# Performance work log

Measured on AMD Instinct MI355X. Metric: run time of the kernel, lower is better.

Reference implementation:

```python
import jax, jax.numpy as jnp
import numpy as np

N = 50000      # nodes
E = 400000     # edges per meta-path
P = 3          # meta-paths
H = 4          # attention heads
D = 32         # hidden_size per head
IN = 128       # in_size = 86 + 42
HD = H * D     # 128
NEG_SLOPE = 0.2


def setup_inputs() -> dict:
    key = jax.random.key(0)
    ks = jax.random.split(key, 13)
    return {
        "h": jax.random.normal(ks[0], (N, 86), dtype=jnp.float32),
        "c_ineigh_feature": jax.random.normal(ks[1], (N, 20, 42), dtype=jnp.float32),
        "fa_w1": jax.random.normal(ks[2], (42, 16), dtype=jnp.float32) * 0.1,
        "fa_b1": jnp.zeros((16,), dtype=jnp.float32),
        "fa_w2": jax.random.normal(ks[3], (16, 1), dtype=jnp.float32) * 0.1,
        "gat_W": jax.random.normal(ks[4], (P, IN, HD), dtype=jnp.float32) * 0.05,
        "attn_l": jax.random.normal(ks[5], (P, H, D), dtype=jnp.float32) * 0.1,
        "attn_r": jax.random.normal(ks[6], (P, H, D), dtype=jnp.float32) * 0.1,
        "sa_w1": jax.random.normal(ks[7], (HD, 128), dtype=jnp.float32) * 0.1,
        "sa_b1": jnp.zeros((128,), dtype=jnp.float32),
        "sa_w2": jax.random.normal(ks[8], (128, 1), dtype=jnp.float32) * 0.1,
        "src": jax.random.randint(ks[9], (P, E), 0, N, dtype=jnp.int32),
        "dst": jax.random.randint(ks[10], (P, E), 0, N, dtype=jnp.int32),
    }


def _gat_conv(x, W, a_l, a_r, s, d):
    """DGL-style GATConv (feat_drop=attn_drop=0, eval mode), activation=elu."""
    feat = (x @ W).reshape(N, H, D)               # [N,H,D]
    el = (feat * a_l).sum(-1)                     # [N,H]
    er = (feat * a_r).sum(-1)                     # [N,H]
    e = el[s] + er[d]                             # [E,H]
    e = jnp.where(e > 0, e, NEG_SLOPE * e)        # leaky_relu(0.2)
    # edge softmax over incoming edges of each dst node
    m = jax.ops.segment_max(e, d, num_segments=N)
    m = jax.lax.stop_gradient(jnp.where(jnp.isfinite(m), m, 0.0))
    ee = jnp.exp(e - m[d])                        # [E,H]
    z = jax.ops.segment_sum(ee, d, num_segments=N)
    alpha = ee / z[d]                             # [E,H]
    msg = alpha[:, :, None] * feat[s]             # [E,H,D]
    out = jax.ops.segment_sum(msg, d, num_segments=N)  # [N,H,D]
    return jax.nn.elu(out).reshape(N, HD)


def reference(h, c_ineigh_feature, fa_w1, fa_b1, fa_w2, gat_W, attn_l, attn_r,
              sa_w1, sa_b1, sa_w2, src, dst):
    # FeatureAttention over the 42-dim neighbor features
    w = jnp.tanh(c_ineigh_feature @ fa_w1 + fa_b1) @ fa_w2   # [N,20,1]
    beta = jax.nn.softmax(w, axis=1)
    c_emb = (beta * c_ineigh_feature).sum(1)                 # [N,42]
    x = jnp.concatenate([h, c_emb], axis=1)                  # [N,128]

    # One GATConv per meta-path
    embs = [_gat_conv(x, gat_W[p], attn_l[p], attn_r[p], src[p], dst[p])
            for p in range(P)]
    z = jnp.stack(embs, axis=1)                              # [N,P,HD]

    # SemanticAttention across meta-paths
    wsem = (jnp.tanh(z @ sa_w1 + sa_b1) @ sa_w2).mean(0)     # [P,1]
    bsem = jax.nn.softmax(wsem, axis=0)                      # [P,1]
    return (bsem[None] * z).sum(1)                           # [N,HD]
```

## Files before the change

### kernel.cpp

```cpp
#include <hip/hip_runtime.h>
#include <hip/hip_bf16.h>

#define NN 50000
#define EE 400000
#define PP 3
#define NBLK 196

__device__ __forceinline__ float eluf(float v) {
    return v > 0.f ? v : (expf(v) - 1.f);
}

__device__ __forceinline__ void fma4(float4& a, float s, const float4& w) {
    a.x += s * w.x; a.y += s * w.y; a.z += s * w.z; a.w += s * w.w;
}

__device__ __forceinline__ unsigned short f2bf(float f) {
    unsigned int u = __float_as_uint(f);
    u = (u + 0x7FFFu + ((u >> 16) & 1u)) >> 16;
    return (unsigned short)u;
}
__device__ __forceinline__ float bf_lo(unsigned int u) { return __uint_as_float(u << 16); }
__device__ __forceinline__ float bf_hi(unsigned int u) { return __uint_as_float(u & 0xFFFF0000u); }

__global__ __launch_bounds__(256) void k_fa_w(
    const float* __restrict__ c, const float* __restrict__ w1,
    const float* __restrict__ b1, const float* __restrict__ w2,
    float* __restrict__ wout)
{
    __shared__ float sW1[42 * 16];
    const int tid = threadIdx.x;
    for (int i = tid; i < 672; i += 256) sW1[i] = w1[i];
    __syncthreads();

    const int t = blockIdx.x * 256 + tid;
    if (t >= NN * 5) return;
    const int n = t / 5;
    const int q = t - 5 * n;

    const float2* base = (const float2*)(c + (size_t)n * 840 + q * 168);
    const float4* sW4 = (const float4*)sW1;

    float4 acc[4][4];
    #pragma unroll
    for (int r = 0; r < 4; ++r)
        #pragma unroll
        for (int jq = 0; jq < 4; ++jq) acc[r][jq] = make_float4(0.f, 0.f, 0.f, 0.f);

    #pragma unroll 3
    for (int i2 = 0; i2 < 21; ++i2) {
        const float4 wa0 = sW4[(2 * i2) * 4 + 0];
        const float4 wa1 = sW4[(2 * i2) * 4 + 1];
        const float4 wa2 = sW4[(2 * i2) * 4 + 2];
        const float4 wa3 = sW4[(2 * i2) * 4 + 3];
        const float4 wb0 = sW4[(2 * i2 + 1) * 4 + 0];
        const float4 wb1 = sW4[(2 * i2 + 1) * 4 + 1];
        const float4 wb2 = sW4[(2 * i2 + 1) * 4 + 2];
        const float4 wb3 = sW4[(2 * i2 + 1) * 4 + 3];
        #pragma unroll
        for (int r = 0; r < 4; ++r) {
            const float2 v = base[r * 21 + i2];
            fma4(acc[r][0], v.x, wa0); fma4(acc[r][1], v.x, wa1);
            fma4(acc[r][2], v.x, wa2); fma4(acc[r][3], v.x, wa3);
            fma4(acc[r][0], v.y, wb0); fma4(acc[r][1], v.y, wb1);
            fma4(acc[r][2], v.y, wb2); fma4(acc[r][3], v.y, wb3);
        }
    }

    float4 bb[4], ww[4];
    #pragma unroll
    for (int jq = 0; jq < 4; ++jq) {
        bb[jq] = ((const float4*)b1)[jq];
        ww[jq] = ((const float4*)w2)[jq];
    }
    float* wo = wout + (size_t)n * 20 + q * 4;
    #pragma unroll
    for (int r = 0; r < 4; ++r) {
        float s = 0.f;
        #pragma unroll
        for (int jq = 0; jq < 4; ++jq) {
            s += tanhf(acc[r][jq].x + bb[jq].x) * ww[jq].x;
            s += tanhf(acc[r][jq].y + bb[jq].y) * ww[jq].y;
            s += tanhf(acc[r][jq].z + bb[jq].z) * ww[jq].z;
            s += tanhf(acc[r][jq].w + bb[jq].w) * ww[jq].w;
        }
        wo[r] = s;
    }
}

__global__ __launch_bounds__(256) void k_fa_emb(
    const float* __restrict__ h, const float* __restrict__ c,
    const float* __restrict__ w, float* __restrict__ x)
{
    const int wid = threadIdx.x >> 6, lane = threadIdx.x & 63;
    const int n = blockIdx.x * 4 + wid;
    if (n >= NN) return;

    const float* wn = w + (size_t)n * 20;
    float wv[20];
    #pragma unroll
    for (int r = 0; r < 20; ++r) wv[r] = wn[r];
    float m = wv[0];
    #pragma unroll
    for (int r = 1; r < 20; ++r) m = fmaxf(m, wv[r]);
    float s = 0.f;
    #pragma unroll
    for (int r = 0; r < 20; ++r) { wv[r] = expf(wv[r] - m); s += wv[r]; }
    const float inv = 1.f / s;

    if (lane < 42) {
        const float* cn = c + (size_t)n * 840;
        float acc = 0.f;
        #pragma unroll
        for (int r = 0; r < 20; ++r) acc += wv[r] * cn[r * 42 + lane];
        x[(size_t)n * 128 + 86 + lane] = acc * inv;
    }
    x[(size_t)n * 128 + lane] = h[(size_t)n * 86 + lane];
    if (lane < 22)
        x[(size_t)n * 128 + 64 + lane] = h[(size_t)n * 86 + 64 + lane];
}

__global__ __launch_bounds__(256) void k_gat_gemm(
    const float* __restrict__ x, const float* __restrict__ W,
    const float* __restrict__ attn_l, const float* __restrict__ attn_r,
    unsigned short* __restrict__ featb, float* __restrict__ el, float* __restrict__ er)
{
    __shared__ float sX[64 * 128];
    const int tid = threadIdx.x;
    const int p  = blockIdx.y;
    const int n0 = blockIdx.x * 64;

    float4* sX4 = (float4*)sX;
    for (int i = tid; i < 2048; i += 256) {
        const int row = i >> 5, c4 = i & 31;
        float4 v = make_float4(0.f, 0.f, 0.f, 0.f);
        if (n0 + row < NN) v = ((const float4*)(x + (size_t)(n0 + row) * 128))[c4];
        sX4[i] = v;
    }
    __syncthreads();

    const int tc = tid & 31;
    const int tr = tid >> 5;
    const float4* Wp4 = (const float4*)(W + (size_t)p * 128 * 128);

    float4 acc[8];
    #pragma unroll
    for (int r = 0; r < 8; ++r) acc[r] = make_float4(0.f, 0.f, 0.f, 0.f);

    for (int kq = 0; kq < 32; ++kq) {
        const float4 wv0 = Wp4[(4 * kq + 0) * 32 + tc];
        const float4 wv1 = Wp4[(4 * kq + 1) * 32 + tc];
        const float4 wv2 = Wp4[(4 * kq + 2) * 32 + tc];
        const float4 wv3 = Wp4[(4 * kq + 3) * 32 + tc];
        #pragma unroll
        for (int r = 0; r < 8; ++r) {
            const float4 xv = sX4[(tr * 8 + r) * 32 + kq];
            fma4(acc[r], xv.x, wv0);
            fma4(acc[r], xv.y, wv1);
            fma4(acc[r], xv.z, wv2);
            fma4(acc[r], xv.w, wv3);
        }
    }

    float4 al, ar;
    {
        al = ((const float4*)(attn_l + p * 128))[tc];
        ar = ((const float4*)(attn_r + p * 128))[tc];
    }
    const int hh = tc >> 3;
    for (int r = 0; r < 8; ++r) {
        const int n = n0 + tr * 8 + r;
        const bool ok = n < NN;
        if (ok) {
            ushort4 sv;
            sv.x = f2bf(acc[r].x); sv.y = f2bf(acc[r].y);
            sv.z = f2bf(acc[r].z); sv.w = f2bf(acc[r].w);
            ((ushort4*)(featb + (size_t)(p * NN + n) * 128))[tc] = sv;
        }
        float pl = acc[r].x*al.x + acc[r].y*al.y + acc[r].z*al.z + acc[r].w*al.w;
        float pr = acc[r].x*ar.x + acc[r].y*ar.y + acc[r].z*ar.z + acc[r].w*ar.w;
        pl += __shfl_xor(pl, 1); pl += __shfl_xor(pl, 2); pl += __shfl_xor(pl, 4);
        pr += __shfl_xor(pr, 1); pr += __shfl_xor(pr, 2); pr += __shfl_xor(pr, 4);
        if (ok && (tc & 7) == 0) {
            el[(size_t)(p * NN + n) * 4 + hh] = pl;
            er[(size_t)(p * NN + n) * 4 + hh] = pr;
        }
    }
}

__global__ __launch_bounds__(256) void k_hist(
    const int* __restrict__ dst, int* __restrict__ deg)
{
    const int p = blockIdx.y;
    const int e = blockIdx.x * 256 + threadIdx.x;
    if (e < EE) atomicAdd(&deg[p * NN + dst[p * EE + e]], 1);
}

__global__ __launch_bounds__(256) void k_partial(
    const int* __restrict__ deg, int* __restrict__ psum)
{
    __shared__ int s[256];
    const int p = blockIdx.y;
    const int i = blockIdx.x * 256 + threadIdx.x;
    s[threadIdx.x] = (i < NN) ? deg[p * NN + i] : 0;
    __syncthreads();
    for (int off = 128; off > 0; off >>= 1) {
        if (threadIdx.x < off) s[threadIdx.x] += s[threadIdx.x + off];
        __syncthreads();
    }
    if (threadIdx.x == 0) psum[p * NBLK + blockIdx.x] = s[0];
}

__global__ void k_scanpsum(int* __restrict__ psum)
{
    const int p = blockIdx.x;
    if (threadIdx.x == 0) {
        int run = 0;
        for (int i = 0; i < NBLK; ++i) {
            int t = psum[p * NBLK + i];
            psum[p * NBLK + i] = run;
            run += t;
        }
    }
}

__global__ __launch_bounds__(256) void k_scanfinal(
    const int* __restrict__ deg, const int* __restrict__ psum,
    int* __restrict__ row_start, int* __restrict__ cursor)
{
    __shared__ int s[256];
    const int p = blockIdx.y, t = threadIdx.x;
    const int i = blockIdx.x * 256 + t;
    const int v = (i < NN) ? deg[p * NN + i] : 0;
    s[t] = v;
    __syncthreads();
    for (int off = 1; off < 256; off <<= 1) {
        int xv = 0;
        if (t >= off) xv = s[t - off];
        __syncthreads();
        s[t] += xv;
        __syncthreads();
    }
    const int excl = s[t] - v + psum[p * NBLK + blockIdx.x];
    if (i < NN) {
        row_start[p * (NN + 1) + i] = excl;
        cursor[p * NN + i] = excl;
        if (i == NN - 1) row_start[p * (NN + 1) + NN] = excl + v;
    }
}

__global__ __launch_bounds__(256) void k_scatter(
    const int* __restrict__ src, const int* __restrict__ dst,
    const float* __restrict__ el, const float* __restrict__ er,
    int* __restrict__ cursor, int* __restrict__ s_src, float* __restrict__ s_ee)
{
    const int p = blockIdx.y;
    const int e = blockIdx.x * 256 + threadIdx.x;
    if (e >= EE) return;
    const int s = src[p * EE + e];
    const int d = dst[p * EE + e];
    const float4 a = ((const float4*)el)[p * NN + s];
    const float4 b = ((const float4*)er)[p * NN + d];
    float4 o;
    {
        float t0 = a.x + b.x, t1 = a.y + b.y, t2 = a.z + b.z, t3 = a.w + b.w;
        t0 = t0 > 0.f ? t0 : 0.2f * t0;
        t1 = t1 > 0.f ? t1 : 0.2f * t1;
        t2 = t2 > 0.f ? t2 : 0.2f * t2;
        t3 = t3 > 0.f ? t3 : 0.2f * t3;
        o = make_float4(expf(t0), expf(t1), expf(t2), expf(t3));
    }
    const int slot = atomicAdd(&cursor[p * NN + d], 1);
    s_src[p * EE + slot] = s;
    ((float4*)s_ee)[p * EE + slot] = o;
}

__global__ __launch_bounds__(256) void k_agg(
    const int* __restrict__ row_start, const int* __restrict__ s_src,
    const float* __restrict__ s_ee, const unsigned short* __restrict__ featb,
    unsigned int* __restrict__ zb)
{
    const int p = blockIdx.y;
    const int w = threadIdx.x >> 6;
    const int lane = threadIdx.x & 63;
    const int n = blockIdx.x * 4 + w;
    if (n >= NN) return;
    const int st = row_start[p * (NN + 1) + n];
    const int en = row_start[p * (NN + 1) + n + 1];

    const int h = lane >> 4;
    const int* ss = s_src + (size_t)p * EE;
    const float4* ee4 = (const float4*)s_ee + (size_t)p * EE;
    const unsigned short* fbase = featb + (size_t)p * NN * 128;

    float acc0 = 0.f, acc1 = 0.f, za = 0.f;
    int i = st;
    for (; i + 4 <= en; i += 4) {
        const int sn0 = ss[i], sn1 = ss[i + 1], sn2 = ss[i + 2], sn3 = ss[i + 3];
        const float4 q0 = ee4[i], q1 = ee4[i + 1], q2 = ee4[i + 2], q3 = ee4[i + 3];
        const unsigned int u0 = ((const unsigned int*)(fbase + (size_t)sn0 * 128))[lane];
        const unsigned int u1 = ((const unsigned int*)(fbase + (size_t)sn1 * 128))[lane];
        const unsigned int u2 = ((const unsigned int*)(fbase + (size_t)sn2 * 128))[lane];
        const unsigned int u3 = ((const unsigned int*)(fbase + (size_t)sn3 * 128))[lane];
        const float e0 = (h < 2) ? (h == 0 ? q0.x : q0.y) : (h == 2 ? q0.z : q0.w);
        const float e1 = (h < 2) ? (h == 0 ? q1.x : q1.y) : (h == 2 ? q1.z : q1.w);
        const float e2 = (h < 2) ? (h == 0 ? q2.x : q2.y) : (h == 2 ? q2.z : q2.w);
        const float e3 = (h < 2) ? (h == 0 ? q3.x : q3.y) : (h == 2 ? q3.z : q3.w);
        acc0 += e0 * bf_lo(u0) + e1 * bf_lo(u1) + e2 * bf_lo(u2) + e3 * bf_lo(u3);
        acc1 += e0 * bf_hi(u0) + e1 * bf_hi(u1) + e2 * bf_hi(u2) + e3 * bf_hi(u3);
        za += (e0 + e1) + (e2 + e3);
    }
    for (; i < en; ++i) {
        const int sn = ss[i];
        const float4 q = ee4[i];
        const unsigned int u = ((const unsigned int*)(fbase + (size_t)sn * 128))[lane];
        const float e = (h < 2) ? (h == 0 ? q.x : q.y) : (h == 2 ? q.z : q.w);
        acc0 += e * bf_lo(u);
        acc1 += e * bf_hi(u);
        za += e;
    }
    float v0 = 0.f, v1 = 0.f;
    if (en > st) { const float iz = 1.f / za; v0 = acc0 * iz; v1 = acc1 * iz; }
    v0 = v0 > 0.f ? v0 : (expf(v0) - 1.f);
    v1 = v1 > 0.f ? v1 : (expf(v1) - 1.f);
    zb[(size_t)(p * NN + n) * 64 + lane] =
        (unsigned int)f2bf(v0) | ((unsigned int)f2bf(v1) << 16);
}

__global__ __launch_bounds__(256) void k_sem_score(
    const unsigned int* __restrict__ zb, const float* __restrict__ w1,
    const float* __restrict__ b1, const float* __restrict__ w2,
    float* __restrict__ wsem)
{
    __shared__ float sZ[64 * 128];
    __shared__ float sPart[8];
    const int tid = threadIdx.x;
    const int p  = blockIdx.y;
    const int n0 = blockIdx.x * 64;

    float4* sZ4 = (float4*)sZ;
    for (int i = tid; i < 2048; i += 256) {
        const int row = i >> 5, c4 = i & 31;
        float4 v = make_float4(0.f, 0.f, 0.f, 0.f);
        if (n0 + row < NN) {
            const uint2 u = ((const uint2*)(zb + (size_t)(p * NN + n0 + row) * 64))[c4];
            v.x = bf_lo(u.x); v.y = bf_hi(u.x); v.z = bf_lo(u.y); v.w = bf_hi(u.y);
        }
        sZ4[i] = v;
    }
    __syncthreads();

    const int tc = tid & 31;
    const int tr = tid >> 5;
    const float4* w14 = (const float4*)w1;

    float4 acc[8];
    #pragma unroll
    for (int r = 0; r < 8; ++r) acc[r] = make_float4(0.f, 0.f, 0.f, 0.f);

    for (int kq = 0; kq < 32; ++kq) {
        const float4 wv0 = w14[(4 * kq + 0) * 32 + tc];
        const float4 wv1 = w14[(4 * kq + 1) * 32 + tc];
        const float4 wv2 = w14[(4 * kq + 2) * 32 + tc];
        const float4 wv3 = w14[(4 * kq + 3) * 32 + tc];
        #pragma unroll
        for (int r = 0; r < 8; ++r) {
            const float4 zv = sZ4[(tr * 8 + r) * 32 + kq];
            fma4(acc[r], zv.x, wv0);
            fma4(acc[r], zv.y, wv1);
            fma4(acc[r], zv.z, wv2);
            fma4(acc[r], zv.w, wv3);
        }
    }

    const float4 bb = ((const float4*)b1)[tc];
    const float4 ww = ((const float4*)w2)[tc];

    float local = 0.f;
    for (int r = 0; r < 8; ++r) {
        float pr = tanhf(acc[r].x + bb.x) * ww.x
                 + tanhf(acc[r].y + bb.y) * ww.y
                 + tanhf(acc[r].z + bb.z) * ww.z
                 + tanhf(acc[r].w + bb.w) * ww.w;
        pr += __shfl_xor(pr, 1);
        pr += __shfl_xor(pr, 2);
        pr += __shfl_xor(pr, 4);
        pr += __shfl_xor(pr, 8);
        pr += __shfl_xor(pr, 16);
        if (tc == 0 && (n0 + tr * 8 + r) < NN) local += pr;
    }
    if (tc == 0) sPart[tr] = local;
    __syncthreads();
    if (tid == 0) {
        float t = 0.f;
        for (int i = 0; i < 8; ++i) t += sPart[i];
        atomicAdd(&wsem[p], t);
    }
}

__global__ void k_bsem(const float* __restrict__ wsem, float* __restrict__ bsem)
{
    if (threadIdx.x == 0 && blockIdx.x == 0) {
        float w[PP];
        for (int p = 0; p < PP; ++p) w[p] = wsem[p] / (float)NN;
        float m = fmaxf(w[0], fmaxf(w[1], w[2]));
        float s = 0.f;
        for (int p = 0; p < PP; ++p) { w[p] = expf(w[p] - m); s += w[p]; }
        for (int p = 0; p < PP; ++p) bsem[p] = w[p] / s;
    }
}

__global__ __launch_bounds__(256) void k_final(
    const unsigned int* __restrict__ zb, const float* __restrict__ bsem,
    float* __restrict__ out)
{
    const int i = blockIdx.x * 256 + threadIdx.x;
    if (i >= NN * 64) return;
    const float b0 = bsem[0], b1 = bsem[1], b2 = bsem[2];
    const unsigned int u0 = zb[i];
    const unsigned int u1 = zb[(size_t)NN * 64 + i];
    const unsigned int u2 = zb[(size_t)2 * NN * 64 + i];
    float2 o;
    o.x = b0 * bf_lo(u0) + b1 * bf_lo(u1) + b2 * bf_lo(u2);
    o.y = b0 * bf_hi(u0) + b1 * bf_hi(u1) + b2 * bf_hi(u2);
    ((float2*)out)[i] = o;
}

extern "C" void kernel_launch(void* const* d_in, const int* in_sizes, int n_in,
                              void* d_out, int out_size, void* d_ws, size_t ws_size,
                              hipStream_t stream) {
    const float* h      = (const float*)d_in[0];
    const float* c      = (const float*)d_in[1];
    const float* fa_w1  = (const float*)d_in[2];
    const float* fa_b1  = (const float*)d_in[3];
    const float* fa_w2  = (const float*)d_in[4];
    const float* gat_W  = (const float*)d_in[5];
    const float* attn_l = (const float*)d_in[6];
    const float* attn_r = (const float*)d_in[7];
    const float* sa_w1  = (const float*)d_in[8];
    const float* sa_b1  = (const float*)d_in[9];
    const float* sa_w2  = (const float*)d_in[10];
    const int*   src    = (const int*)d_in[11];
    const int*   dst    = (const int*)d_in[12];
    float* out = (float*)d_out;

    float* ws = (float*)d_ws;
    float* x     = ws;
    int*   s_src = (int*)ws;
    float* s_ee  = ws + 1200000;
    float* w_fa  = ws + 6400000;
    unsigned short* featb = (unsigned short*)(ws + 7400000);
    float* el    = ws + 17000000;
    float* er    = el + 600000;
    unsigned int* zb = (unsigned int*)(er + 600000);
    int*   row_start = (int*)(ws + 27800000);
    int*   cursor    = row_start + 150003;
    int*   psum      = cursor + 150000;
    int*   deg       = psum + 588;
    float* wsem      = (float*)(deg + 150000);
    float* bsem      = wsem + 4;

    hipMemsetAsync(deg, 0, (size_t)(150000 + 4) * sizeof(float), stream);

    k_fa_w<<<(NN * 5 + 255) / 256, 256, 0, stream>>>(c, fa_w1, fa_b1, fa_w2, w_fa);
    k_fa_emb<<<(NN + 3) / 4, 256, 0, stream>>>(h, c, w_fa, x);
    k_gat_gemm<<<dim3((NN + 63) / 64, PP), 256, 0, stream>>>(x, gat_W, attn_l, attn_r, featb, el, er);
    k_hist<<<dim3((EE + 255) / 256, PP), 256, 0, stream>>>(dst, deg);
    k_partial<<<dim3(NBLK, PP), 256, 0, stream>>>(deg, psum);
    k_scanpsum<<<PP, 64, 0, stream>>>(psum);
    k_scanfinal<<<dim3(NBLK, PP), 256, 0, stream>>>(deg, psum, row_start, cursor);
    k_scatter<<<dim3((EE + 255) / 256, PP), 256, 0, stream>>>(src, dst, el, er, cursor, s_src, s_ee);
    k_agg<<<dim3((NN + 3) / 4, PP), 256, 0, stream>>>(row_start, s_src, s_ee, featb, zb);
    k_sem_score<<<dim3((NN + 63) / 64, PP), 256, 0, stream>>>(zb, sa_w1, sa_b1, sa_w2, wsem);
    k_bsem<<<1, 64, 0, stream>>>(wsem, bsem);
    k_final<<<(NN * 64 + 255) / 256, 256, 0, stream>>>(zb, bsem, out);
}
```

Measured before the change: 824.7 us.

## Fuse feature-attention score and embedding kernels, staging neighbor features in LDS

Merges the two feature-attention kernels into one. Each wavefront loads one node's 20x42 neighbor features into shared memory once, computes the tanh-MLP scores, reduces them with shuffles, and then reuses the staged features for the weighted sum. This removes the second global read of the 168MB feature tensor and the intermediate score buffer round trip. In exchange, per-thread compute is reorganised and LDS use per block rises, which may reduce occupancy.

```diff
diff --git a/kernel.cpp b/kernel.cpp
--- a/kernel.cpp
+++ b/kernel.cpp
@@ -22,83 +22,61 @@
 __device__ __forceinline__ float bf_lo(unsigned int u) { return __uint_as_float(u << 16); }
 __device__ __forceinline__ float bf_hi(unsigned int u) { return __uint_as_float(u & 0xFFFF0000u); }
 
-__global__ __launch_bounds__(256) void k_fa_w(
-    const float* __restrict__ c, const float* __restrict__ w1,
-    const float* __restrict__ b1, const float* __restrict__ w2,
-    float* __restrict__ wout)
-{
-    __shared__ float sW1[42 * 16];
+__global__ __launch_bounds__(256) void k_fa(
+    const float* __restrict__ h, const float* __restrict__ c,
+    const float* __restrict__ w1, const float* __restrict__ b1,
+    const float* __restrict__ w2, float* __restrict__ x)
+{
+    __shared__ float sC[4][840];
+    __shared__ float sW1[672];
+    __shared__ float sWr[4][20];
     const int tid = threadIdx.x;
+    const int wid = tid >> 6, lane = tid & 63;
+    const int n = blockIdx.x * 4 + wid;
+
     for (int i = tid; i < 672; i += 256) sW1[i] = w1[i];
-    __syncthreads();
-
-    const int t = blockIdx.x * 256 + tid;
-    if (t >= NN * 5) return;
-    const int n = t / 5;
-    const int q = t - 5 * n;
-
-    const float2* base = (const float2*)(c + (size_t)n * 840 + q * 168);
-    const float4* sW4 = (const float4*)sW1;
-
-    float4 acc[4][4];
-    #pragma unroll
-    for (int r = 0; r < 4; ++r)
-        #pragma unroll
-        for (int jq = 0; jq < 4; ++jq) acc[r][jq] = make_float4(0.f, 0.f, 0.f, 0.f);
-
-    #pragma unroll 3
-    for (int i2 = 0; i2 < 21; ++i2) {
-        const float4 wa0 = sW4[(2 * i2) * 4 + 0];
-        const float4 wa1 = sW4[(2 * i2) * 4 + 1];
-        const float4 wa2 = sW4[(2 * i2) * 4 + 2];
-        const float4 wa3 = sW4[(2 * i2) * 4 + 3];
-        const float4 wb0 = sW4[(2 * i2 + 1) * 4 + 0];
-        const float4 wb1 = sW4[(2 * i2 + 1) * 4 + 1];
-        const float4 wb2 = sW4[(2 * i2 + 1) * 4 + 2];
-        const float4 wb3 = sW4[(2 * i2 + 1) * 4 + 3];
-        #pragma unroll
-        for (int r = 0; r < 4; ++r) {
-            const float2 v = base[r * 21 + i2];
-            fma4(acc[r][0], v.x, wa0); fma4(acc[r][1], v.x, wa1);
-            fma4(acc[r][2], v.x, wa2); fma4(acc[r][3], v.x, wa3);
-            fma4(acc[r][0], v.y, wb0); fma4(acc[r][1], v.y, wb1);
-            fma4(acc[r][2], v.y, wb2); fma4(acc[r][3], v.y, wb3);
-        }
-    }
-
-    float4 bb[4], ww[4];
-    #pragma unroll
-    for (int jq = 0; jq < 4; ++jq) {
-        bb[jq] = ((const float4*)b1)[jq];
-        ww[jq] = ((const float4*)w2)[jq];
-    }
-    float* wo = wout + (size_t)n * 20 + q * 4;
-    #pragma unroll
-    for (int r = 0; r < 4; ++r) {
-        float s = 0.f;
-        #pragma unroll
-        for (int jq = 0; jq < 4; ++jq) {
-            s += tanhf(acc[r][jq].x + bb[jq].x) * ww[jq].x;
-            s += tanhf(acc[r][jq].y + bb[jq].y) * ww[jq].y;
-            s += tanhf(acc[r][jq].z + bb[jq].z) * ww[jq].z;
-            s += tanhf(acc[r][jq].w + bb[jq].w) * ww[jq].w;
-        }
-        wo[r] = s;
-    }
-}
-
-__global__ __launch_bounds__(256) void k_fa_emb(
-    const float* __restrict__ h, const float* __restrict__ c,
-    const float* __restrict__ w, float* __restrict__ x)
-{
-    const int wid = threadIdx.x >> 6, lane = threadIdx.x & 63;
-    const int n = blockIdx.x * 4 + wid;
+
+    if (n < NN) {
+        const float4* cn4 = (const float4*)(c + (size_t)n * 840);
+        float4* sC4 = (float4*)sC[wid];
+        #pragma unroll
+        for (int k = lane; k < 210; k += 64) sC4[k] = cn4[k];
+    }
+    __syncthreads();
+
+    const int j = lane & 15, rg = lane >> 4;
+    if (n < NN) {
+        const float bj = b1[j], w2j = w2[j];
+        float pr[5];
+        #pragma unroll
+        for (int rr = 0; rr < 5; ++rr) {
+            const int r = rg * 5 + rr;
+            float acc = bj;
+            const float* row = &sC[wid][r * 42];
+            #pragma unroll
+            for (int i = 0; i < 42; ++i) acc += row[i] * sW1[i * 16 + j];
+            pr[rr] = tanhf(acc) * w2j;
+        }
+        #pragma unroll
+        for (int rr = 0; rr < 5; ++rr) {
+            float v = pr[rr];
+            v += __shfl_xor(v, 1);
+            v += __shfl_xor(v, 2);
+            v += __shfl_xor(v, 4);
+            v += __shfl_xor(v, 8);
+            pr[rr] = v;
+        }
+        if (j == 0) {
+            #pragma unroll
+            for (int rr = 0; rr < 5; ++rr) sWr[wid][rg * 5 + rr] = pr[rr];
+        }
+    }
+    __syncthreads();
+
     if (n >= NN) return;
-
-    const float* wn = w + (size_t)n * 20;
     float wv[20];
     #pragma unroll
-    for (int r = 0; r < 20; ++r) wv[r] = wn[r];
+    for (int r = 0; r < 20; ++r) wv[r] = sWr[wid][r];
     float m = wv[0];
     #pragma unroll
     for (int r = 1; r < 20; ++r) m = fmaxf(m, wv[r]);
@@ -108,10 +86,9 @@
     const float inv = 1.f / s;
 
     if (lane < 42) {
-        const float* cn = c + (size_t)n * 840;
         float acc = 0.f;
         #pragma unroll
-        for (int r = 0; r < 20; ++r) acc += wv[r] * cn[r * 42 + lane];
+        for (int r = 0; r < 20; ++r) acc += wv[r] * sC[wid][r * 42 + lane];
         x[(size_t)n * 128 + 86 + lane] = acc * inv;
     }
     x[(size_t)n * 128 + lane] = h[(size_t)n * 86 + lane];
@@ -447,7 +424,6 @@
     float* x     = ws;
     int*   s_src = (int*)ws;
     float* s_ee  = ws + 1200000;
-    float* w_fa  = ws + 6400000;
     unsigned short* featb = (unsigned short*)(ws + 7400000);
     float* el    = ws + 17000000;
     float* er    = el + 600000;
@@ -461,8 +437,7 @@
 
     hipMemsetAsync(deg, 0, (size_t)(150000 + 4) * sizeof(float), stream);
 
-    k_fa_w<<<(NN * 5 + 255) / 256, 256, 0, stream>>>(c, fa_w1, fa_b1, fa_w2, w_fa);
-    k_fa_emb<<<(NN + 3) / 4, 256, 0, stream>>>(h, c, w_fa, x);
+    k_fa<<<(NN + 3) / 4, 256, 0, stream>>>(h, c, fa_w1, fa_b1, fa_w2, x);
     k_gat_gemm<<<dim3((NN + 63) / 64, PP), 256, 0, stream>>>(x, gat_W, attn_l, attn_r, featb, el, er);
     k_hist<<<dim3((EE + 255) / 256, PP), 256, 0, stream>>>(dst, deg);
     k_partial<<<dim3(NBLK, PP), 256, 0, stream>>>(deg, psum);
```

Measured after the change: 716.5 us. -13.1%, faster.
